# Optimization experiments

Hardware: AMD Instinct MI355X
Metric: run time of the kernel (lower is better)

Reference implementation:

```python
import jax, jax.numpy as jnp
import numpy as np

N_NODES = 50000
N_EDGES = 800000

def _graph_conv(x, W, b, src, dst, n_nodes):
    # DGL GraphConv, norm='both': D_dst^{-1/2} * A * D_src^{-1/2} * X * W + b
    ones_e = jnp.ones((src.shape[0],), dtype=x.dtype)
    deg_out = jax.ops.segment_sum(ones_e, src, num_segments=n_nodes)
    deg_in = jax.ops.segment_sum(ones_e, dst, num_segments=n_nodes)
    norm_src = jnp.maximum(deg_out, 1.0) ** -0.5  # [N]
    norm_dst = jnp.maximum(deg_in, 1.0) ** -0.5   # [N]
    xs = x * norm_src[:, None]                    # pre-normalize
    agg = jax.ops.segment_sum(xs[src], dst, num_segments=n_nodes)  # SpMM
    agg = agg * norm_dst[:, None]
    return agg @ W + b

def setup_inputs() -> dict:
    key = jax.random.key(0)
    k1, k2, k3, k4, k5 = jax.random.split(key, 5)
    features = jax.random.normal(k1, (N_NODES, 128), dtype=jnp.float32)
    W1 = jax.random.normal(k2, (128, 256), dtype=jnp.float32) * (1.0 / np.sqrt(128))
    b1 = jnp.zeros((256,), dtype=jnp.float32)
    W2 = jax.random.normal(k3, (256, 40), dtype=jnp.float32) * (1.0 / np.sqrt(256))
    b2 = jnp.zeros((40,), dtype=jnp.float32)
    src = jax.random.randint(k4, (N_EDGES,), 0, N_NODES, dtype=jnp.int32)
    dst = jax.random.randint(k5, (N_EDGES,), 0, N_NODES, dtype=jnp.int32)
    return {"features": features, "W1": W1, "b1": b1, "W2": W2, "b2": b2,
            "src": src, "dst": dst}

def reference(features, W1, b1, W2, b2, src, dst):
    n = features.shape[0]
    # layer 1: GraphConv with activation=relu, then an extra F.relu (idempotent)
    h = _graph_conv(features, W1, b1, src, dst, n)
    h = jax.nn.relu(h)
    # dropout(p=0.5): identity in eval mode (deterministic reference)
    h = _graph_conv(h, W2, b2, src, dst, n)
    return jax.nn.log_softmax(h, axis=1)
```

## Files before the change

kernel.cpp:

```cpp
#include <hip/hip_runtime.h>
#include <cstdint>
#include <cstddef>

#define N_NODES 50000
#define N_EDGES 800000
#define F_IN    128
#define F_HID   256
#define F_OUT   40
#define NB      196

__global__ __launch_bounds__(256) void degree_kernel(
    const int* __restrict__ src, const int* __restrict__ dst,
    int* __restrict__ deg_out, int* __restrict__ deg_in) {
  int i = blockIdx.x * 256 + threadIdx.x;
  if (i < N_EDGES) {
    atomicAdd(&deg_out[src[i]], 1);
    atomicAdd(&deg_in[dst[i]], 1);
  }
}

__global__ __launch_bounds__(256) void block_sum_kernel(
    const int* __restrict__ deg_in, int* __restrict__ bsum) {
  __shared__ int arr[256];
  int node = blockIdx.x * 256 + threadIdx.x;
  arr[threadIdx.x] = (node < N_NODES) ? deg_in[node] : 0;
  __syncthreads();
  for (int off = 128; off > 0; off >>= 1) {
    if (threadIdx.x < off) arr[threadIdx.x] += arr[threadIdx.x + off];
    __syncthreads();
  }
  if (threadIdx.x == 0) bsum[blockIdx.x] = arr[0];
}

__global__ __launch_bounds__(256) void scan_bsum_kernel(int* __restrict__ bsum) {
  __shared__ int arr[256];
  int tid = threadIdx.x;
  int v = (tid < NB) ? bsum[tid] : 0;
  arr[tid] = v;
  __syncthreads();
  for (int off = 1; off < 256; off <<= 1) {
    int t = (tid >= off) ? arr[tid - off] : 0;
    __syncthreads();
    arr[tid] += t;
    __syncthreads();
  }
  if (tid < NB) bsum[tid] = arr[tid] - v;
}

__global__ __launch_bounds__(256) void finalize_kernel(
    const int* __restrict__ deg_out, const int* __restrict__ deg_in,
    const int* __restrict__ bsum, int* __restrict__ row_ptr,
    int* __restrict__ cursor, float* __restrict__ norm_src,
    float* __restrict__ norm_dst) {
  __shared__ int arr[256];
  int tid = threadIdx.x;
  int node = blockIdx.x * 256 + tid;
  int di = (node < N_NODES) ? deg_in[node] : 0;
  arr[tid] = di;
  __syncthreads();
  for (int off = 1; off < 256; off <<= 1) {
    int t = (tid >= off) ? arr[tid - off] : 0;
    __syncthreads();
    arr[tid] += t;
    __syncthreads();
  }
  if (node < N_NODES) {
    int rp = bsum[blockIdx.x] + arr[tid] - di;
    row_ptr[node] = rp;
    cursor[node] = rp;
    norm_dst[node] = 1.0f / sqrtf(fmaxf((float)di, 1.0f));
    norm_src[node] = 1.0f / sqrtf(fmaxf((float)deg_out[node], 1.0f));
  }
  if (blockIdx.x == 0 && tid == 0) row_ptr[N_NODES] = N_EDGES;
}

__global__ __launch_bounds__(256) void scatter_kernel(
    const int* __restrict__ src, const int* __restrict__ dst,
    int* __restrict__ cursor, int* __restrict__ csr_src) {
  int i = blockIdx.x * 256 + threadIdx.x;
  if (i < N_EDGES) {
    int d = dst[i];
    int p = atomicAdd(&cursor[d], 1);
    csr_src[p] = src[i];
  }
}

__global__ __launch_bounds__(256) void prescale_kernel(
    const float* __restrict__ feat, const float* __restrict__ norm_src,
    float* __restrict__ xs) {
  int i = blockIdx.x * 256 + threadIdx.x;
  int row = i >> 5;
  float4 v = ((const float4*)feat)[i];
  float ns = norm_src[row];
  v.x *= ns; v.y *= ns; v.z *= ns; v.w *= ns;
  ((float4*)xs)[i] = v;
}

__global__ __launch_bounds__(256) void agg1_kernel(
    const float* __restrict__ xs, const int* __restrict__ row_ptr,
    const int* __restrict__ csr_src, const float* __restrict__ norm_dst,
    float* __restrict__ out) {
  int wid = (blockIdx.x * 256 + threadIdx.x) >> 6;
  if (wid >= N_NODES) return;
  int lane = threadIdx.x & 63;
  int g = lane >> 5;
  int l32 = lane & 31;
  int beg = row_ptr[wid], end = row_ptr[wid + 1];
  float4 acc = make_float4(0.f, 0.f, 0.f, 0.f);
  int e = beg + g;
  if (e < end) {
    int s = csr_src[e];
    while (true) {
      int en = e + 2;
      int sn = (en < end) ? csr_src[en] : 0;
      float4 f = *(const float4*)(xs + (size_t)s * F_IN + (l32 << 2));
      acc.x += f.x; acc.y += f.y; acc.z += f.z; acc.w += f.w;
      if (en >= end) break;
      e = en; s = sn;
    }
  }
  acc.x += __shfl_xor(acc.x, 32);
  acc.y += __shfl_xor(acc.y, 32);
  acc.z += __shfl_xor(acc.z, 32);
  acc.w += __shfl_xor(acc.w, 32);
  if (g == 0) {
    float nd = norm_dst[wid];
    acc.x *= nd; acc.y *= nd; acc.z *= nd; acc.w *= nd;
    *(float4*)(out + (size_t)wid * F_IN + (l32 << 2)) = acc;
  }
}

__global__ __launch_bounds__(256) void gemm1_kernel(
    const float* __restrict__ A, const float* __restrict__ B,
    const float* __restrict__ bias, float* __restrict__ C, int M) {
  constexpr int BM = 128, BN = 64, BK = 32, TM = 8, TN = 4;
  constexpr int N = F_HID, K = F_IN;
  __shared__ float As[BK][BM + 4];
  __shared__ float Bs[BK][BN];
  int tid = threadIdx.x;
  int tx = tid % (BN / TN);
  int ty = tid / (BN / TN);
  int row0 = blockIdx.x * BM;
  int col0 = blockIdx.y * BN;
  float acc[TM][TN];
#pragma unroll
  for (int i = 0; i < TM; ++i)
#pragma unroll
    for (int j = 0; j < TN; ++j) acc[i][j] = 0.f;

  for (int k0 = 0; k0 < K; k0 += BK) {
#pragma unroll
    for (int idx = tid; idx < BM * BK / 4; idx += 256) {
      int r = idx / (BK / 4);
      int c4 = idx % (BK / 4);
      int row = row0 + r;
      float4 v = (row < M) ? *(const float4*)(A + (size_t)row * K + k0 + c4 * 4)
                           : make_float4(0.f, 0.f, 0.f, 0.f);
      As[c4 * 4 + 0][r] = v.x;
      As[c4 * 4 + 1][r] = v.y;
      As[c4 * 4 + 2][r] = v.z;
      As[c4 * 4 + 3][r] = v.w;
    }
#pragma unroll
    for (int idx = tid; idx < BK * BN / 4; idx += 256) {
      int r = idx / (BN / 4);
      int c4 = idx % (BN / 4);
      *(float4*)(&Bs[r][c4 * 4]) =
          *(const float4*)(B + (size_t)(k0 + r) * N + col0 + c4 * 4);
    }
    __syncthreads();
#pragma unroll
    for (int k = 0; k < BK; ++k) {
      float4 a0 = *(const float4*)(&As[k][ty * TM]);
      float4 a1 = *(const float4*)(&As[k][ty * TM + 4]);
      float4 b0 = *(const float4*)(&Bs[k][tx * TN]);
      float a[TM] = {a0.x, a0.y, a0.z, a0.w, a1.x, a1.y, a1.z, a1.w};
      float b[TN] = {b0.x, b0.y, b0.z, b0.w};
#pragma unroll
      for (int i = 0; i < TM; ++i)
#pragma unroll
        for (int j = 0; j < TN; ++j) acc[i][j] += a[i] * b[j];
    }
    __syncthreads();
  }

#pragma unroll
  for (int i = 0; i < TM; ++i) {
    int row = row0 + ty * TM + i;
    if (row >= M) continue;
    float4 bv = *(const float4*)(bias + col0 + tx * TN);
    float4 v = make_float4(fmaxf(acc[i][0] + bv.x, 0.f),
                           fmaxf(acc[i][1] + bv.y, 0.f),
                           fmaxf(acc[i][2] + bv.z, 0.f),
                           fmaxf(acc[i][3] + bv.w, 0.f));
    *(float4*)(C + (size_t)row * N + col0 + tx * TN) = v;
  }
}

__global__ __launch_bounds__(320) void gemm2_kernel(
    const float* __restrict__ A, const float* __restrict__ B,
    const float* __restrict__ rowscale, float* __restrict__ C, int M) {
  constexpr int BM = 128, BN = 40, BK = 32, TM = 4, TN = 4;
  constexpr int N = F_OUT, K = F_HID;
  __shared__ float As[BK][BM + 4];
  __shared__ float Bs[BK][BN];
  int tid = threadIdx.x;
  int tx = tid % (BN / TN);
  int ty = tid / (BN / TN);
  int row0 = blockIdx.x * BM;
  float acc[TM][TN];
#pragma unroll
  for (int i = 0; i < TM; ++i)
#pragma unroll
    for (int j = 0; j < TN; ++j) acc[i][j] = 0.f;

  for (int k0 = 0; k0 < K; k0 += BK) {
    for (int idx = tid; idx < BM * BK / 4; idx += 320) {
      int r = idx / (BK / 4);
      int c4 = idx % (BK / 4);
      int row = row0 + r;
      float4 v = (row < M) ? *(const float4*)(A + (size_t)row * K + k0 + c4 * 4)
                           : make_float4(0.f, 0.f, 0.f, 0.f);
      As[c4 * 4 + 0][r] = v.x;
      As[c4 * 4 + 1][r] = v.y;
      As[c4 * 4 + 2][r] = v.z;
      As[c4 * 4 + 3][r] = v.w;
    }
    {
      int r = tid / 10;
      int c4 = tid % 10;
      *(float4*)(&Bs[r][c4 * 4]) =
          *(const float4*)(B + (size_t)(k0 + r) * N + c4 * 4);
    }
    __syncthreads();
#pragma unroll
    for (int k = 0; k < BK; ++k) {
      float4 a0 = *(const float4*)(&As[k][ty * TM]);
      float4 b0 = *(const float4*)(&Bs[k][tx * TN]);
      float a[TM] = {a0.x, a0.y, a0.z, a0.w};
      float b[TN] = {b0.x, b0.y, b0.z, b0.w};
#pragma unroll
      for (int i = 0; i < TM; ++i)
#pragma unroll
        for (int j = 0; j < TN; ++j) acc[i][j] += a[i] * b[j];
    }
    __syncthreads();
  }

#pragma unroll
  for (int i = 0; i < TM; ++i) {
    int row = row0 + ty * TM + i;
    if (row >= M) continue;
    float rs = rowscale[row];
    float4 v = make_float4(acc[i][0] * rs, acc[i][1] * rs,
                           acc[i][2] * rs, acc[i][3] * rs);
    *(float4*)(C + (size_t)row * N + tx * TN) = v;
  }
}

__global__ __launch_bounds__(256) void agg2_softmax_kernel(
    const float* __restrict__ t, const int* __restrict__ row_ptr,
    const int* __restrict__ csr_src, const float* __restrict__ norm_dst,
    const float* __restrict__ b2, float* __restrict__ out) {
  int wid = (blockIdx.x * 256 + threadIdx.x) >> 6;
  if (wid >= N_NODES) return;
  int lane = threadIdx.x & 63;
  int g = lane >> 4;
  int l16 = lane & 15;
  bool act = l16 < 10;
  int beg = row_ptr[wid], end = row_ptr[wid + 1];
  float4 acc = make_float4(0.f, 0.f, 0.f, 0.f);
  for (int e = beg + g; e < end; e += 4) {
    int s = csr_src[e];
    if (act) {
      float4 f = *(const float4*)(t + (size_t)s * F_OUT + (l16 << 2));
      acc.x += f.x; acc.y += f.y; acc.z += f.z; acc.w += f.w;
    }
  }
#pragma unroll
  for (int off = 16; off <= 32; off <<= 1) {
    acc.x += __shfl_xor(acc.x, off);
    acc.y += __shfl_xor(acc.y, off);
    acc.z += __shfl_xor(acc.z, off);
    acc.w += __shfl_xor(acc.w, off);
  }
  float nd = norm_dst[wid];
  float4 v;
  if (act) {
    float4 bv = *(const float4*)(b2 + (l16 << 2));
    v = make_float4(acc.x * nd + bv.x, acc.y * nd + bv.y,
                    acc.z * nd + bv.z, acc.w * nd + bv.w);
  } else {
    v = make_float4(-INFINITY, -INFINITY, -INFINITY, -INFINITY);
  }
  float m = fmaxf(fmaxf(v.x, v.y), fmaxf(v.z, v.w));
#pragma unroll
  for (int off = 1; off <= 8; off <<= 1) m = fmaxf(m, __shfl_xor(m, off));
  float ex = act ? (expf(v.x - m) + expf(v.y - m) + expf(v.z - m) + expf(v.w - m)) : 0.f;
#pragma unroll
  for (int off = 1; off <= 8; off <<= 1) ex += __shfl_xor(ex, off);
  float ls = logf(ex);
  if (g == 0 && act) {
    float4 r = make_float4(v.x - m - ls, v.y - m - ls, v.z - m - ls, v.w - m - ls);
    *(float4*)(out + (size_t)wid * F_OUT + (l16 << 2)) = r;
  }
}

extern "C" void kernel_launch(void* const* d_in, const int* in_sizes, int n_in,
                              void* d_out, int out_size, void* d_ws, size_t ws_size,
                              hipStream_t stream) {
  const float* feat = (const float*)d_in[0];
  const float* W1   = (const float*)d_in[1];
  const float* b1   = (const float*)d_in[2];
  const float* W2   = (const float*)d_in[3];
  const float* b2   = (const float*)d_in[4];
  const int*   src  = (const int*)d_in[5];
  const int*   dst  = (const int*)d_in[6];
  float* out = (float*)d_out;

  char* p = (char*)d_ws;
  auto alloc = [&](size_t bytes) {
    char* r = p;
    p += (bytes + 255) & ~(size_t)255;
    return r;
  };
  int*   deg_out  = (int*)alloc((size_t)N_NODES * 4);
  int*   deg_in   = (int*)alloc((size_t)N_NODES * 4);
  int*   bsum     = (int*)alloc((size_t)NB * 4);
  int*   row_ptr  = (int*)alloc((size_t)(N_NODES + 1) * 4);
  int*   cursor   = (int*)alloc((size_t)N_NODES * 4);
  int*   csr_src  = (int*)alloc((size_t)N_EDGES * 4);
  float* norm_src = (float*)alloc((size_t)N_NODES * 4);
  float* norm_dst = (float*)alloc((size_t)N_NODES * 4);
  float* t        = (float*)alloc((size_t)N_NODES * F_OUT * 4);
  float* xs       = (float*)alloc((size_t)N_NODES * F_HID * 4);
  float* h        = xs;
  float* agg1     = (float*)alloc((size_t)N_NODES * F_IN * 4);

  size_t zero_bytes = (size_t)((char*)bsum - (char*)deg_out);
  hipMemsetAsync(deg_out, 0, zero_bytes, stream);

  degree_kernel<<<(N_EDGES + 255) / 256, 256, 0, stream>>>(src, dst, deg_out, deg_in);
  block_sum_kernel<<<NB, 256, 0, stream>>>(deg_in, bsum);
  scan_bsum_kernel<<<1, 256, 0, stream>>>(bsum);
  finalize_kernel<<<NB, 256, 0, stream>>>(deg_out, deg_in, bsum, row_ptr, cursor,
                                          norm_src, norm_dst);
  scatter_kernel<<<(N_EDGES + 255) / 256, 256, 0, stream>>>(src, dst, cursor, csr_src);
  prescale_kernel<<<N_NODES * (F_IN / 4) / 256, 256, 0, stream>>>(feat, norm_src, xs);
  agg1_kernel<<<(N_NODES * 64) / 256 + 1, 256, 0, stream>>>(xs, row_ptr, csr_src,
                                                            norm_dst, agg1);
  gemm1_kernel<<<dim3((N_NODES + 127) / 128, F_HID / 64), 256, 0, stream>>>(
      agg1, W1, b1, h, N_NODES);
  gemm2_kernel<<<(N_NODES + 127) / 128, 320, 0, stream>>>(h, W2, norm_src, t, N_NODES);
  agg2_softmax_kernel<<<(N_NODES * 64) / 256 + 1, 256, 0, stream>>>(
      t, row_ptr, csr_src, norm_dst, b2, out);
}
```

Before: 381.9 us.

## Privatize degree and scatter cursors into eight replicated copies

Degree counting and CSR scatter now spread their atomics over eight copies of the counters, picked by block index, to cut atomic contention. A new reduce kernel sums the copies, and finalize hands each copy its own sub-range of row offsets. This costs more memset traffic (about 3.2 MB zeroed instead of 0.4 MB), an extra kernel launch and extra reads. Atomic contention was already low, since edges are spread randomly over 50k nodes.

After: 383.1 us. About the same (+0.3%).

```diff
diff --git a/kernel.cpp b/kernel.cpp
--- a/kernel.cpp
+++ b/kernel.cpp
@@ -8,15 +8,36 @@
 #define F_HID   256
 #define F_OUT   40
 #define NB      196
+#define NCOPY   8
+#define SREP    50176
 
 __global__ __launch_bounds__(256) void degree_kernel(
     const int* __restrict__ src, const int* __restrict__ dst,
-    int* __restrict__ deg_out, int* __restrict__ deg_in) {
-  int i = blockIdx.x * 256 + threadIdx.x;
+    int* __restrict__ degc_out, int* __restrict__ degc_in) {
+  int b = blockIdx.x;
+  int i = b * 256 + threadIdx.x;
+  int k = b & (NCOPY - 1);
   if (i < N_EDGES) {
-    atomicAdd(&deg_out[src[i]], 1);
-    atomicAdd(&deg_in[dst[i]], 1);
-  }
+    atomicAdd(&degc_out[k * SREP + src[i]], 1);
+    atomicAdd(&degc_in[k * SREP + dst[i]], 1);
+  }
+}
+
+__global__ __launch_bounds__(256) void reduce_kernel(
+    const int* __restrict__ degc_out, const int* __restrict__ degc_in,
+    int* __restrict__ deg_in_tot, float* __restrict__ norm_src,
+    float* __restrict__ norm_dst) {
+  int v = blockIdx.x * 256 + threadIdx.x;
+  if (v >= N_NODES) return;
+  int di = 0, dq = 0;
+#pragma unroll
+  for (int k = 0; k < NCOPY; ++k) {
+    di += degc_in[k * SREP + v];
+    dq += degc_out[k * SREP + v];
+  }
+  deg_in_tot[v] = di;
+  norm_dst[v] = 1.0f / sqrtf(fmaxf((float)di, 1.0f));
+  norm_src[v] = 1.0f / sqrtf(fmaxf((float)dq, 1.0f));
 }
 
 __global__ __launch_bounds__(256) void block_sum_kernel(
@@ -48,14 +69,13 @@
 }
 
 __global__ __launch_bounds__(256) void finalize_kernel(
-    const int* __restrict__ deg_out, const int* __restrict__ deg_in,
+    const int* __restrict__ deg_in_tot, const int* __restrict__ degc_in,
     const int* __restrict__ bsum, int* __restrict__ row_ptr,
-    int* __restrict__ cursor, float* __restrict__ norm_src,
-    float* __restrict__ norm_dst) {
+    int* __restrict__ cur) {
   __shared__ int arr[256];
   int tid = threadIdx.x;
   int node = blockIdx.x * 256 + tid;
-  int di = (node < N_NODES) ? deg_in[node] : 0;
+  int di = (node < N_NODES) ? deg_in_tot[node] : 0;
   arr[tid] = di;
   __syncthreads();
   for (int off = 1; off < 256; off <<= 1) {
@@ -67,20 +87,25 @@
   if (node < N_NODES) {
     int rp = bsum[blockIdx.x] + arr[tid] - di;
     row_ptr[node] = rp;
-    cursor[node] = rp;
-    norm_dst[node] = 1.0f / sqrtf(fmaxf((float)di, 1.0f));
-    norm_src[node] = 1.0f / sqrtf(fmaxf((float)deg_out[node], 1.0f));
+    int b = rp;
+#pragma unroll
+    for (int k = 0; k < NCOPY; ++k) {
+      cur[k * SREP + node] = b;
+      b += degc_in[k * SREP + node];
+    }
   }
   if (blockIdx.x == 0 && tid == 0) row_ptr[N_NODES] = N_EDGES;
 }
 
 __global__ __launch_bounds__(256) void scatter_kernel(
     const int* __restrict__ src, const int* __restrict__ dst,
-    int* __restrict__ cursor, int* __restrict__ csr_src) {
-  int i = blockIdx.x * 256 + threadIdx.x;
+    int* __restrict__ cur, int* __restrict__ csr_src) {
+  int b = blockIdx.x;
+  int i = b * 256 + threadIdx.x;
+  int k = b & (NCOPY - 1);
   if (i < N_EDGES) {
     int d = dst[i];
-    int p = atomicAdd(&cursor[d], 1);
+    int p = atomicAdd(&cur[k * SREP + d], 1);
     csr_src[p] = src[i];
   }
 }
@@ -324,11 +349,12 @@
     p += (bytes + 255) & ~(size_t)255;
     return r;
   };
-  int*   deg_out  = (int*)alloc((size_t)N_NODES * 4);
-  int*   deg_in   = (int*)alloc((size_t)N_NODES * 4);
+  int*   degc_out = (int*)alloc((size_t)NCOPY * SREP * 4);
+  int*   degc_in  = (int*)alloc((size_t)NCOPY * SREP * 4);
+  int*   cur      = (int*)alloc((size_t)NCOPY * SREP * 4);
+  int*   deg_in_tot = (int*)alloc((size_t)N_NODES * 4);
   int*   bsum     = (int*)alloc((size_t)NB * 4);
   int*   row_ptr  = (int*)alloc((size_t)(N_NODES + 1) * 4);
-  int*   cursor   = (int*)alloc((size_t)N_NODES * 4);
   int*   csr_src  = (int*)alloc((size_t)N_EDGES * 4);
   float* norm_src = (float*)alloc((size_t)N_NODES * 4);
   float* norm_dst = (float*)alloc((size_t)N_NODES * 4);
@@ -337,15 +363,15 @@
   float* h        = xs;
   float* agg1     = (float*)alloc((size_t)N_NODES * F_IN * 4);
 
-  size_t zero_bytes = (size_t)((char*)bsum - (char*)deg_out);
-  hipMemsetAsync(deg_out, 0, zero_bytes, stream);
-
-  degree_kernel<<<(N_EDGES + 255) / 256, 256, 0, stream>>>(src, dst, deg_out, deg_in);
-  block_sum_kernel<<<NB, 256, 0, stream>>>(deg_in, bsum);
+  size_t zero_bytes = (size_t)((char*)cur - (char*)degc_out);
+  hipMemsetAsync(degc_out, 0, zero_bytes, stream);
+
+  degree_kernel<<<(N_EDGES + 255) / 256, 256, 0, stream>>>(src, dst, degc_out, degc_in);
+  reduce_kernel<<<NB, 256, 0, stream>>>(degc_out, degc_in, deg_in_tot, norm_src, norm_dst);
+  block_sum_kernel<<<NB, 256, 0, stream>>>(deg_in_tot, bsum);
   scan_bsum_kernel<<<1, 256, 0, stream>>>(bsum);
-  finalize_kernel<<<NB, 256, 0, stream>>>(deg_out, deg_in, bsum, row_ptr, cursor,
-                                          norm_src, norm_dst);
-  scatter_kernel<<<(N_EDGES + 255) / 256, 256, 0, stream>>>(src, dst, cursor, csr_src);
+  finalize_kernel<<<NB, 256, 0, stream>>>(deg_in_tot, degc_in, bsum, row_ptr, cur);
+  scatter_kernel<<<(N_EDGES + 255) / 256, 256, 0, stream>>>(src, dst, cur, csr_src);
   prescale_kernel<<<N_NODES * (F_IN / 4) / 256, 256, 0, stream>>>(feat, norm_src, xs);
   agg1_kernel<<<(N_NODES * 64) / 256 + 1, 256, 0, stream>>>(xs, row_ptr, csr_src,
                                                             norm_dst, agg1);
```
